# Optimization experiments

Hardware: AMD Instinct MI355X
Metric: run time of the kernel (lower is better)

## Reference

```python
import jax, jax.numpy as jnp
import numpy as np

GRAPH_SIZE = 512  # N: graph_size from init


def setup_inputs() -> dict:
    key = jax.random.key(0)
    k1, k2 = jax.random.split(key)
    B, N, C_IN, C_OUT = 128, GRAPH_SIZE, 128, 128
    # X packs [adjacency | features] along last dim, matching the torch forward
    X = jax.random.uniform(k1, (B, N, N + C_IN), dtype=jnp.float32)
    W = jax.random.normal(k2, (C_IN, C_OUT), dtype=jnp.float32)
    return {"X": X, "W": W}


def reference(X, W):
    N = GRAPH_SIZE
    A = X[:, :, :N]            # [B, N, N] dense adjacency
    feat = X[:, :, N:]         # [B, N, C_in]
    # D = diag(rowsum(A)); pinv(D).sqrt() == diag(1/sqrt(deg)) with 0 where deg==0
    deg = jnp.sum(A, axis=2)   # [B, N]
    d_inv_sqrt = jnp.where(deg > 0, 1.0 / jnp.sqrt(deg), 0.0)
    A_hat = A + jnp.eye(N, dtype=A.dtype)  # A + I
    # D^-1/2 @ A_hat @ D^-1/2 as elementwise row/col scaling (diag matmuls)
    A_norm = d_inv_sqrt[:, :, None] * A_hat * d_inv_sqrt[:, None, :]
    # relu(A_norm @ X @ W)
    h = jnp.einsum('bnm,bmf->bnf', A_norm, feat)
    out = jax.nn.relu(jnp.einsum('bnf,fo->bno', h, W))
    return jnp.concatenate([A, out], axis=2)  # [B, N, N + C_out]
```

## Files before the change

kernel.cpp:

```cpp
#include <hip/hip_runtime.h>
#include <stdint.h>

#define GS   512
#define CF   128
#define XROW 640
#define NB   128

typedef __attribute__((ext_vector_type(4))) float          f32x4;
typedef __attribute__((ext_vector_type(8))) short          s16x8;
typedef __attribute__((ext_vector_type(4))) unsigned short u16x4;
typedef __attribute__((ext_vector_type(8))) unsigned short u16x8;

__device__ __forceinline__ unsigned short f2bf(float f) {
    unsigned u = __builtin_bit_cast(unsigned, f);
    u = (u + 0x7fffu + ((u >> 16) & 1u)) >> 16;
    return (unsigned short)u;
}
__device__ __forceinline__ float bf2f(unsigned short h) {
    unsigned u = ((unsigned)h) << 16;
    return __builtin_bit_cast(float, u);
}
__device__ __forceinline__ void glds16(const void* g, void* l) {
    __builtin_amdgcn_global_load_lds(
        (const __attribute__((address_space(1))) void*)g,
        (__attribute__((address_space(3))) void*)l, 16, 0, 0);
}

__global__ __launch_bounds__(256) void k0_wt(const float* __restrict__ W,
                                             unsigned short* __restrict__ WTst) {
    const int e = blockIdx.x * 256 + threadIdx.x;
    const int j = e & 7, f = (e >> 3) & 127, q = e >> 10;
    const int c = (q >> 2) * 32 + (q & 3) * 8 + j;
    WTst[e] = f2bf(W[c * CF + f]);
}

__global__ __launch_bounds__(256) void k1_pre(const float* __restrict__ X,
                                              float* __restrict__ out,
                                              float* __restrict__ dis,
                                              unsigned short* __restrict__ Abf) {
    const int wv = threadIdx.x >> 6, l = threadIdx.x & 63;
    const int gbase = blockIdx.x << 3;
#pragma unroll
    for (int p = 0; p < 2; ++p) {
        const int gr = gbase + wv + (p << 2);
        const f32x4* rp = (const f32x4*)(X + (size_t)gr * XROW);
        f32x4* op = (f32x4*)(out + (size_t)gr * XROW);
        f32x4 v0 = rp[2 * l], v1 = rp[2 * l + 1];
        op[2 * l] = v0; op[2 * l + 1] = v1;
        u16x8 o;
        o[0] = f2bf(v0[0]); o[1] = f2bf(v0[1]); o[2] = f2bf(v0[2]); o[3] = f2bf(v0[3]);
        o[4] = f2bf(v1[0]); o[5] = f2bf(v1[1]); o[6] = f2bf(v1[2]); o[7] = f2bf(v1[3]);
        *(u16x8*)((char*)Abf + ((size_t)gr << 10) + (l << 4)) = o;
        float s = (v0[0] + v0[1]) + (v0[2] + v0[3]) + (v1[0] + v1[1]) + (v1[2] + v1[3]);
#pragma unroll
        for (int off = 32; off; off >>= 1) s += __shfl_xor(s, off, 64);
        if (l == 0) dis[gr] = (s > 0.f) ? (1.f / sqrtf(s)) : 0.f;
    }
}

__global__ __launch_bounds__(256) void k2_featw(const float* __restrict__ X,
                                                const unsigned short* __restrict__ WTst,
                                                const float* __restrict__ dis,
                                                unsigned short* __restrict__ fwdT) {
    __shared__ __align__(16) float sf[64 * 128];
    __shared__ __align__(16) unsigned short swt[16384];
    const int t = threadIdx.x, l = t & 63, wv = t >> 6;
    const int m0 = blockIdx.x << 6;
    const int b = m0 >> 9, ml0 = m0 & (GS - 1);

    const char* fb = (const char*)(X + (size_t)m0 * XROW + GS);
    char* sfb = (char*)sf;
#pragma unroll
    for (int it = 0; it < 8; ++it) {
        int chunk = it * 256 + t;
        int row = chunk >> 5, c16 = chunk & 31;
        int c16s = c16 ^ (row & 7);
        glds16(fb + (size_t)row * (XROW * 4) + c16s * 16, sfb + it * 4096 + wv * 1024);
    }
#pragma unroll
    for (int it = 0; it < 8; ++it)
        glds16((const char*)WTst + it * 4096 + wv * 1024 + l * 16,
               (char*)swt + it * 4096 + wv * 1024);
    __syncthreads();

    const int wr = wv >> 1, wc = wv & 1, lr = l & 15, lk = l >> 4;
    f32x4 acc[2][4];
#pragma unroll
    for (int i = 0; i < 2; ++i)
#pragma unroll
        for (int j = 0; j < 4; ++j)
#pragma unroll
            for (int r = 0; r < 4; ++r) acc[i][j][r] = 0.f;

#pragma unroll
    for (int ks = 0; ks < 4; ++ks) {
        s16x8 af[2];
#pragma unroll
        for (int i = 0; i < 2; ++i) {
            int row = (wr << 5) + (i << 4) + lr;
            int cb = (ks << 3) + (lk << 1);
            int c0 = cb ^ (row & 7), c1 = (cb + 1) ^ (row & 7);
            f32x4 x0 = *(const f32x4*)&sf[row * 128 + (c0 << 2)];
            f32x4 x1 = *(const f32x4*)&sf[row * 128 + (c1 << 2)];
            s16x8 a;
            a[0] = f2bf(x0[0]); a[1] = f2bf(x0[1]); a[2] = f2bf(x0[2]); a[3] = f2bf(x0[3]);
            a[4] = f2bf(x1[0]); a[5] = f2bf(x1[1]); a[6] = f2bf(x1[2]); a[7] = f2bf(x1[3]);
            af[i] = a;
        }
#pragma unroll
        for (int j = 0; j < 4; ++j) {
            int f = (wc << 6) + (j << 4) + lr;
            s16x8 bfr = *(const s16x8*)&swt[((((ks << 2) | lk) << 7) | f) << 3];
#pragma unroll
            for (int i = 0; i < 2; ++i)
                acc[i][j] = __builtin_amdgcn_mfma_f32_16x16x32_bf16(af[i], bfr, acc[i][j], 0, 0, 0);
        }
    }

#pragma unroll
    for (int i = 0; i < 2; ++i) {
        int mr = (wr << 5) + (i << 4) + (lk << 2);
        f32x4 d4 = *(const f32x4*)&dis[m0 + mr];
        int mg = ml0 + mr;
        int ktm = mg >> 5, q3 = (mg >> 3) & 3, jm = mg & 7;
#pragma unroll
        for (int j = 0; j < 4; ++j) {
            int f = (wc << 6) + (j << 4) + lr;
            u16x4 o;
            o[0] = f2bf(d4[0] * acc[i][j][0]);
            o[1] = f2bf(d4[1] * acc[i][j][1]);
            o[2] = f2bf(d4[2] * acc[i][j][2]);
            o[3] = f2bf(d4[3] * acc[i][j][3]);
            *(u16x4*)((char*)fwdT + ((size_t)b << 17) + (((ktm << 2) | q3) << 11)
                      + (f << 4) + (jm << 1)) = o;
        }
    }
}

__global__ __launch_bounds__(256) void k3_gcn(const unsigned short* __restrict__ Abf,
                                              const float* __restrict__ dis,
                                              const unsigned short* __restrict__ fwdT,
                                              float* __restrict__ out) {
    __shared__ __align__(16) unsigned short sb[2][8192];
    const int t = threadIdx.x, l = t & 63, wv = t >> 6, lr = l & 15, lk = l >> 4;
    const int b = blockIdx.x >> 3, bm0 = (blockIdx.x & 7) << 6;
    const char* Bt = (const char*)fwdT + ((size_t)b << 17);
    const char* Ab = (const char*)Abf
        + (((size_t)(b * GS + bm0 + (wv << 4) + lr)) << 10) + (lk << 4);

    auto stage = [&](int buf, int ph) {
#pragma unroll
        for (int it = 0; it < 4; ++it)
            glds16(Bt + (ph << 14) + it * 4096 + wv * 1024 + l * 16,
                   (char*)sb[buf] + it * 4096 + wv * 1024);
    };

    f32x4 acc[8];
#pragma unroll
    for (int j = 0; j < 8; ++j)
#pragma unroll
        for (int r = 0; r < 4; ++r) acc[j][r] = 0.f;

    stage(0, 0);
    s16x8 a0 = *(const s16x8*)(Ab);
    s16x8 a1 = *(const s16x8*)(Ab + 64);
    int cur = 0;
    for (int ph = 0; ph < 8; ++ph) {
        __syncthreads();
        if (ph < 7) stage(cur ^ 1, ph + 1);
        s16x8 n0 = a0, n1 = a1;
        if (ph < 7) {
            n0 = *(const s16x8*)(Ab + ((2 * ph + 2) << 6));
            n1 = *(const s16x8*)(Ab + ((2 * ph + 3) << 6));
        }
        __builtin_amdgcn_s_setprio(1);
#pragma unroll
        for (int j = 0; j < 8; ++j) {
            s16x8 bfr = *(const s16x8*)&sb[cur][(lk << 10) + (j << 7) + (lr << 3)];
            acc[j] = __builtin_amdgcn_mfma_f32_16x16x32_bf16(a0, bfr, acc[j], 0, 0, 0);
        }
#pragma unroll
        for (int j = 0; j < 8; ++j) {
            s16x8 bfr = *(const s16x8*)&sb[cur][4096 + (lk << 10) + (j << 7) + (lr << 3)];
            acc[j] = __builtin_amdgcn_mfma_f32_16x16x32_bf16(a1, bfr, acc[j], 0, 0, 0);
        }
        __builtin_amdgcn_s_setprio(0);
        a0 = n0; a1 = n1; cur ^= 1;
    }

    const int n0r = bm0 + (wv << 4) + (lk << 2);
    f32x4 d4 = *(const f32x4*)&dis[(b << 9) + n0r];
    const int ktm = n0r >> 5, q3 = (n0r >> 3) & 3, jm = n0r & 7;
#pragma unroll
    for (int j = 0; j < 8; ++j) {
        int f = (j << 4) + lr;
        u16x4 fw = *(const u16x4*)(Bt + (((ktm << 2) | q3) << 11) + (f << 4) + (jm << 1));
        float* ob = out + ((size_t)(b * GS + n0r)) * XROW + GS + f;
#pragma unroll
        for (int r = 0; r < 4; ++r) {
            float v = d4[r] * (acc[j][r] + bf2f(fw[r]));
            ob[(size_t)r * XROW] = v > 0.f ? v : 0.f;
        }
    }
}

extern "C" void kernel_launch(void* const* d_in, const int* in_sizes, int n_in,
                              void* d_out, int out_size, void* d_ws, size_t ws_size,
                              hipStream_t stream) {
    const float* X = (const float*)d_in[0];
    const float* W = (const float*)d_in[1];
    float* out = (float*)d_out;
    float*          dis  = (float*)d_ws;
    unsigned short* WTst = (unsigned short*)((char*)d_ws + 262144);
    unsigned short* fwdT = (unsigned short*)((char*)d_ws + 294912);
    unsigned short* Abf  = (unsigned short*)((char*)d_ws + 17072128);

    hipLaunchKernelGGL(k0_wt,   dim3(64),   dim3(256), 0, stream, W, WTst);
    hipLaunchKernelGGL(k1_pre,  dim3(NB * GS / 8),  dim3(256), 0, stream, X, out, dis, Abf);
    hipLaunchKernelGGL(k2_featw, dim3(NB * GS / 64), dim3(256), 0, stream, X, WTst, dis, fwdT);
    hipLaunchKernelGGL(k3_gcn,  dim3(NB * GS / 64), dim3(256), 0, stream, Abf, dis, fwdT, out);
}
```

Baseline: 335.4 us.

## Fuse adjacency preprocessing and feature-weight GEMM into one kernel

Merges the adjacency copy/bf16 conversion/degree kernel with the feature×W MFMA kernel. Each block now streams its 64 rows once, converts the feature part to bf16 directly into swizzled LDS, and keeps the inverse-sqrt degrees in LDS, so the feature columns are not re-read from global and one launch disappears. It also removes the s_setprio bracketing around the MFMA loop in the GCN kernel. The cost is fewer blocks (64 rows per block instead of 8) for the memory-bound copy phase, which may reduce latency hiding.

```diff
diff --git a/kernel.cpp b/kernel.cpp
--- a/kernel.cpp
+++ b/kernel.cpp
@@ -34,53 +34,52 @@
     WTst[e] = f2bf(W[c * CF + f]);
 }
 
-__global__ __launch_bounds__(256) void k1_pre(const float* __restrict__ X,
-                                              float* __restrict__ out,
-                                              float* __restrict__ dis,
-                                              unsigned short* __restrict__ Abf) {
-    const int wv = threadIdx.x >> 6, l = threadIdx.x & 63;
-    const int gbase = blockIdx.x << 3;
-#pragma unroll
-    for (int p = 0; p < 2; ++p) {
-        const int gr = gbase + wv + (p << 2);
+__global__ __launch_bounds__(256) void k12(const float* __restrict__ X,
+                                           const unsigned short* __restrict__ WTst,
+                                           float* __restrict__ out,
+                                           float* __restrict__ dis,
+                                           unsigned short* __restrict__ Abf,
+                                           unsigned short* __restrict__ fwdT) {
+    __shared__ __align__(16) unsigned short sfb[64 * 128];
+    __shared__ __align__(16) unsigned short swt[16384];
+    __shared__ __align__(16) float sdis[64];
+    const int t = threadIdx.x, l = t & 63, wv = t >> 6;
+    const int m0 = blockIdx.x << 6;
+    const int b = m0 >> 9, ml0 = m0 & (GS - 1);
+
+#pragma unroll
+    for (int it = 0; it < 8; ++it)
+        glds16((const char*)WTst + it * 4096 + wv * 1024 + l * 16,
+               (char*)swt + it * 4096 + wv * 1024);
+
+    for (int p = 0; p < 16; ++p) {
+        const int rw = (p << 2) + wv;
+        const int gr = m0 + rw;
         const f32x4* rp = (const f32x4*)(X + (size_t)gr * XROW);
+        f32x4 v0 = rp[2 * l], v1 = rp[2 * l + 1];
+        f32x4 vf;
+        if (l < 32) vf = rp[128 + l];
         f32x4* op = (f32x4*)(out + (size_t)gr * XROW);
-        f32x4 v0 = rp[2 * l], v1 = rp[2 * l + 1];
         op[2 * l] = v0; op[2 * l + 1] = v1;
         u16x8 o;
         o[0] = f2bf(v0[0]); o[1] = f2bf(v0[1]); o[2] = f2bf(v0[2]); o[3] = f2bf(v0[3]);
         o[4] = f2bf(v1[0]); o[5] = f2bf(v1[1]); o[6] = f2bf(v1[2]); o[7] = f2bf(v1[3]);
         *(u16x8*)((char*)Abf + ((size_t)gr << 10) + (l << 4)) = o;
+        if (l < 32) {
+            u16x4 fo;
+            fo[0] = f2bf(vf[0]); fo[1] = f2bf(vf[1]); fo[2] = f2bf(vf[2]); fo[3] = f2bf(vf[3]);
+            int ad = (rw << 8) + (l << 3);
+            ad ^= (rw & 7) << 4;
+            *(u16x4*)((char*)sfb + ad) = fo;
+        }
         float s = (v0[0] + v0[1]) + (v0[2] + v0[3]) + (v1[0] + v1[1]) + (v1[2] + v1[3]);
 #pragma unroll
         for (int off = 32; off; off >>= 1) s += __shfl_xor(s, off, 64);
-        if (l == 0) dis[gr] = (s > 0.f) ? (1.f / sqrtf(s)) : 0.f;
-    }
-}
-
-__global__ __launch_bounds__(256) void k2_featw(const float* __restrict__ X,
-                                                const unsigned short* __restrict__ WTst,
-                                                const float* __restrict__ dis,
-                                                unsigned short* __restrict__ fwdT) {
-    __shared__ __align__(16) float sf[64 * 128];
-    __shared__ __align__(16) unsigned short swt[16384];
-    const int t = threadIdx.x, l = t & 63, wv = t >> 6;
-    const int m0 = blockIdx.x << 6;
-    const int b = m0 >> 9, ml0 = m0 & (GS - 1);
-
-    const char* fb = (const char*)(X + (size_t)m0 * XROW + GS);
-    char* sfb = (char*)sf;
-#pragma unroll
-    for (int it = 0; it < 8; ++it) {
-        int chunk = it * 256 + t;
-        int row = chunk >> 5, c16 = chunk & 31;
-        int c16s = c16 ^ (row & 7);
-        glds16(fb + (size_t)row * (XROW * 4) + c16s * 16, sfb + it * 4096 + wv * 1024);
-    }
-#pragma unroll
-    for (int it = 0; it < 8; ++it)
-        glds16((const char*)WTst + it * 4096 + wv * 1024 + l * 16,
-               (char*)swt + it * 4096 + wv * 1024);
+        if (l == 0) {
+            float d = (s > 0.f) ? (1.f / sqrtf(s)) : 0.f;
+            sdis[rw] = d; dis[gr] = d;
+        }
+    }
     __syncthreads();
 
     const int wr = wv >> 1, wc = wv & 1, lr = l & 15, lk = l >> 4;
@@ -98,14 +97,9 @@
 #pragma unroll
         for (int i = 0; i < 2; ++i) {
             int row = (wr << 5) + (i << 4) + lr;
-            int cb = (ks << 3) + (lk << 1);
-            int c0 = cb ^ (row & 7), c1 = (cb + 1) ^ (row & 7);
-            f32x4 x0 = *(const f32x4*)&sf[row * 128 + (c0 << 2)];
-            f32x4 x1 = *(const f32x4*)&sf[row * 128 + (c1 << 2)];
-            s16x8 a;
-            a[0] = f2bf(x0[0]); a[1] = f2bf(x0[1]); a[2] = f2bf(x0[2]); a[3] = f2bf(x0[3]);
-            a[4] = f2bf(x1[0]); a[5] = f2bf(x1[1]); a[6] = f2bf(x1[2]); a[7] = f2bf(x1[3]);
-            af[i] = a;
+            int ad = (row << 8) + (((ks << 2) | lk) << 4);
+            ad ^= (row & 7) << 4;
+            af[i] = *(const s16x8*)((char*)sfb + ad);
         }
 #pragma unroll
         for (int j = 0; j < 4; ++j) {
@@ -120,7 +114,7 @@
 #pragma unroll
     for (int i = 0; i < 2; ++i) {
         int mr = (wr << 5) + (i << 4) + (lk << 2);
-        f32x4 d4 = *(const f32x4*)&dis[m0 + mr];
+        f32x4 d4 = *(const f32x4*)&sdis[mr];
         int mg = ml0 + mr;
         int ktm = mg >> 5, q3 = (mg >> 3) & 3, jm = mg & 7;
 #pragma unroll
@@ -173,7 +167,6 @@
             n0 = *(const s16x8*)(Ab + ((2 * ph + 2) << 6));
             n1 = *(const s16x8*)(Ab + ((2 * ph + 3) << 6));
         }
-        __builtin_amdgcn_s_setprio(1);
 #pragma unroll
         for (int j = 0; j < 8; ++j) {
             s16x8 bfr = *(const s16x8*)&sb[cur][(lk << 10) + (j << 7) + (lr << 3)];
@@ -184,7 +177,6 @@
             s16x8 bfr = *(const s16x8*)&sb[cur][4096 + (lk << 10) + (j << 7) + (lr << 3)];
             acc[j] = __builtin_amdgcn_mfma_f32_16x16x32_bf16(a1, bfr, acc[j], 0, 0, 0);
         }
-        __builtin_amdgcn_s_setprio(0);
         a0 = n0; a1 = n1; cur ^= 1;
     }
 
@@ -215,8 +207,7 @@
     unsigned short* fwdT = (unsigned short*)((char*)d_ws + 294912);
     unsigned short* Abf  = (unsigned short*)((char*)d_ws + 17072128);
 
-    hipLaunchKernelGGL(k0_wt,   dim3(64),   dim3(256), 0, stream, W, WTst);
-    hipLaunchKernelGGL(k1_pre,  dim3(NB * GS / 8),  dim3(256), 0, stream, X, out, dis, Abf);
-    hipLaunchKernelGGL(k2_featw, dim3(NB * GS / 64), dim3(256), 0, stream, X, WTst, dis, fwdT);
-    hipLaunchKernelGGL(k3_gcn,  dim3(NB * GS / 64), dim3(256), 0, stream, Abf, dis, fwdT, out);
-}
+    hipLaunchKernelGGL(k0_wt, dim3(64),            dim3(256), 0, stream, W, WTst);
+    hipLaunchKernelGGL(k12,   dim3(NB * GS / 64),  dim3(256), 0, stream, X, WTst, out, dis, Abf, fwdT);
+    hipLaunchKernelGGL(k3_gcn, dim3(NB * GS / 64), dim3(256), 0, stream, Abf, dis, fwdT, out);
+}
```

Result: no change. 340.2 us (+1.4%).
